# Kernel tuning notes

Measured on AMD Instinct MI355X. Metric: run time of the kernel, lower is better.

## Reference

```python
import jax, jax.numpy as jnp
import numpy as np
import math

D_MODEL = 1024
N_HEADS = 16
HEAD_DIM = D_MODEL // N_HEADS
BATCH = 2
SEQ = 2048


def setup_inputs() -> dict:
    key = jax.random.key(0)
    ks = jax.random.split(key, 6)
    x = jax.random.normal(ks[0], (BATCH, SEQ, D_MODEL), dtype=jnp.float32)
    # causal additive mask, finite large negative
    causal = jnp.tril(jnp.ones((SEQ, SEQ), dtype=bool))
    attn_mask = jnp.where(causal, 0.0, -1e9).astype(jnp.float32)[None, None, :, :]
    s = 1.0 / math.sqrt(D_MODEL)
    W_qkv = jax.random.uniform(ks[1], (3 * D_MODEL, D_MODEL), jnp.float32, -s, s)
    b_qkv = jax.random.uniform(ks[2], (3 * D_MODEL,), jnp.float32, -s, s)
    W_out = jax.random.uniform(ks[3], (D_MODEL, D_MODEL), jnp.float32, -s, s)
    b_out = jax.random.uniform(ks[4], (D_MODEL,), jnp.float32, -s, s)
    return {"x": x, "attn_mask": attn_mask, "W_qkv": W_qkv, "b_qkv": b_qkv,
            "W_out": W_out, "b_out": b_out}


def reference(x, attn_mask, W_qkv, b_qkv, W_out, b_out):
    batch, seq, _ = x.shape
    # torch Linear: x @ W^T + b
    qkv = x @ W_qkv.T + b_qkv                              # [B,S,3D]
    qkv = qkv.reshape(batch, seq, 3, N_HEADS, HEAD_DIM)
    qkv = jnp.transpose(qkv, (2, 0, 3, 1, 4))              # [3,B,H,S,hd]
    q, k, v = qkv[0], qkv[1], qkv[2]
    scores = jnp.einsum('bhsd,bhtd->bhst', q, k) / math.sqrt(HEAD_DIM)
    scores = scores + attn_mask
    attn = jax.nn.softmax(scores, axis=-1)                 # dropout p=0 (eval)
    context = jnp.einsum('bhst,bhtd->bhsd', attn, v)       # [B,H,S,hd]
    context = jnp.transpose(context, (0, 2, 1, 3)).reshape(batch, seq, D_MODEL)
    return context @ W_out.T + b_out
```

## Files before the change

kernel.cpp:

```cpp
#include <hip/hip_runtime.h>
#include <hip/hip_bf16.h>

#define BATCH 2
#define SEQ 2048
#define DMODEL 1024
#define NHEADS 16
#define HDIM 64
#define MROWS (BATCH*SEQ)

typedef short bf16x8_t __attribute__((ext_vector_type(8)));
typedef float f32x4_t __attribute__((ext_vector_type(4)));

union Frag { uint4 u; bf16x8_t b; };

__device__ __forceinline__ unsigned short f2bf(float f) {
  union { __hip_bfloat16 h; unsigned short s; } u;
  u.h = __float2bfloat16(f);
  return u.s;
}

__device__ __forceinline__ void gload16(const unsigned short* g, unsigned short* l) {
  __builtin_amdgcn_global_load_lds(
      (const __attribute__((address_space(1))) unsigned int*)(const void*)g,
      (__attribute__((address_space(3))) unsigned int*)(void*)l,
      16, 0, 0);
}

__global__ void cvt3_kernel(const float* __restrict__ a, const float* __restrict__ b,
                            const float* __restrict__ c,
                            unsigned short* __restrict__ oa, unsigned short* __restrict__ ob,
                            unsigned short* __restrict__ oc,
                            int na, int nb, int nc) {
  const int n = na + nb + nc;
  for (int i = blockIdx.x * blockDim.x + threadIdx.x; i < n;
       i += gridDim.x * blockDim.x) {
    const float* src; unsigned short* dst; int j;
    if (i < na)           { src = a; dst = oa; j = i; }
    else if (i < na + nb) { src = b; dst = ob; j = i - na; }
    else                  { src = c; dst = oc; j = i - na - nb; }
    float4 v = reinterpret_cast<const float4*>(src)[j];
    ushort4 o;
    o.x = f2bf(v.x); o.y = f2bf(v.y); o.z = f2bf(v.z); o.w = f2bf(v.w);
    reinterpret_cast<ushort4*>(dst)[j] = o;
  }
}

#define QSCALE 0.18033688011112042f


__launch_bounds__(256)
__global__ void qkv_gemm_kernel(const unsigned short* __restrict__ A,
                                const unsigned short* __restrict__ Bw,
                                const float* __restrict__ bias,
                                unsigned short* __restrict__ qb,
                                unsigned short* __restrict__ kb,
                                unsigned short* __restrict__ vb) {
  __shared__ __align__(16) unsigned short As[3 * 4096];
  __shared__ __align__(16) unsigned short Bs[3 * 4096];
  const int tid = threadIdx.x;
  const int w = tid >> 6, lane = tid & 63;
  const int rr = lane & 15, cg = lane >> 4;
  const int wr = w >> 1, wc = w & 1;
  const int kswz = (rr >> 1) & 3;
  const int bm = blockIdx.x * 128, bn = blockIdx.y * 128;

  const int cid0 = (w * 2) * 64 + lane, cid1 = (w * 2 + 1) * 64 + lane;
  const int rowA0 = cid0 >> 2, kc0 = (cid0 & 3) ^ ((cid0 >> 3) & 3);
  const int rowA1 = cid1 >> 2, kc1 = (cid1 & 3) ^ ((cid1 >> 3) & 3);
  const unsigned short* gA0 = A + (size_t)(bm + rowA0) * DMODEL + kc0 * 8;
  const unsigned short* gA1 = A + (size_t)(bm + rowA1) * DMODEL + kc1 * 8;
  const unsigned short* gB0 = Bw + (size_t)(bn + rowA0) * DMODEL + kc0 * 8;
  const unsigned short* gB1 = Bw + (size_t)(bn + rowA1) * DMODEL + kc1 * 8;
  unsigned short* lA0 = As + (w * 2) * 512;
  unsigned short* lA1 = As + (w * 2 + 1) * 512;
  unsigned short* lB0 = Bs + (w * 2) * 512;
  unsigned short* lB1 = Bs + (w * 2 + 1) * 512;

#define GSTAGE(bi_, k0_) do {                       \
    gload16(gA0 + (k0_), lA0 + (bi_) * 4096);       \
    gload16(gA1 + (k0_), lA1 + (bi_) * 4096);       \
    gload16(gB0 + (k0_), lB0 + (bi_) * 4096);       \
    gload16(gB1 + (k0_), lB1 + (bi_) * 4096);       \
  } while (0)

  f32x4_t acc[4][4];
#pragma unroll
  for (int i = 0; i < 4; ++i)
#pragma unroll
    for (int j = 0; j < 4; ++j) acc[i][j] = (f32x4_t){0.f, 0.f, 0.f, 0.f};

  GSTAGE(0, 0);
  GSTAGE(1, 32);
  int cur = 0;
  for (int it = 0; it < 32; ++it) {
    if (it < 31) asm volatile("s_waitcnt vmcnt(4)" ::: "memory");
    else         asm volatile("s_waitcnt vmcnt(0)" ::: "memory");
    __builtin_amdgcn_sched_barrier(0);
    __builtin_amdgcn_s_barrier();
    __builtin_amdgcn_sched_barrier(0);
    if (it + 2 < 32) {
      int nb2 = cur + 2; if (nb2 >= 3) nb2 -= 3;
      GSTAGE(nb2, (it + 2) * 32);
    }
    const uint4* A4 = reinterpret_cast<const uint4*>(As) + cur * 512;
    const uint4* B4 = reinterpret_cast<const uint4*>(Bs) + cur * 512;
    Frag af[4], bf[4];
#pragma unroll
    for (int mt = 0; mt < 4; ++mt)
      af[mt].u = A4[(wr * 64 + 16 * mt + rr) * 4 + (cg ^ kswz)];
#pragma unroll
    for (int nt = 0; nt < 4; ++nt)
      bf[nt].u = B4[(wc * 64 + 16 * nt + rr) * 4 + (cg ^ kswz)];
    __builtin_amdgcn_s_setprio(1);
#pragma unroll
    for (int mt = 0; mt < 4; ++mt)
#pragma unroll
      for (int nt = 0; nt < 4; ++nt)
        acc[mt][nt] = __builtin_amdgcn_mfma_f32_16x16x32_bf16(af[mt].b, bf[nt].b, acc[mt][nt], 0, 0, 0);
    __builtin_amdgcn_s_setprio(0);
    cur = (cur == 2) ? 0 : cur + 1;
  }
#undef GSTAGE

#pragma unroll
  for (int nt = 0; nt < 4; ++nt) {
    const int m = bn + wc * 64 + 16 * nt + rr;
    const float bv = bias[m];
    const int which = m >> 10;
    const int h = (m & 1023) >> 6;
    const int d = m & 63;
#pragma unroll
    for (int mt = 0; mt < 4; ++mt) {
#pragma unroll
      for (int r = 0; r < 4; ++r) {
        const int n = bm + wr * 64 + 16 * mt + cg * 4 + r;
        const int b = n >> 11, sq = n & (SEQ - 1);
        const int bh = b * NHEADS + h;
        float val = acc[mt][nt][r] + bv;
        if (which == 0) {
          qb[((size_t)bh * SEQ + sq) * HDIM + d] = f2bf(val * QSCALE);
        } else if (which == 1) {
          kb[((size_t)bh * SEQ + sq) * HDIM + d] = f2bf(val);
        } else {
          vb[((size_t)bh * HDIM + d) * SEQ + sq] = f2bf(val);
        }
      }
    }
  }
}

__launch_bounds__(256)
__global__ void out_gemm_kernel(const unsigned short* __restrict__ A,
                                const unsigned short* __restrict__ Bw,
                                const float* __restrict__ bias,
                                float* __restrict__ out) {
  __shared__ __align__(16) unsigned short As[3 * 4096];
  __shared__ __align__(16) unsigned short Bs[3 * 4096];
  const int tid = threadIdx.x;
  const int w = tid >> 6, lane = tid & 63;
  const int rr = lane & 15, cg = lane >> 4;
  const int wr = w >> 1, wc = w & 1;
  const int kswz = (rr >> 1) & 3;
  const int bm = blockIdx.x * 128, bn = blockIdx.y * 128;

  const int cid0 = (w * 2) * 64 + lane, cid1 = (w * 2 + 1) * 64 + lane;
  const int rowA0 = cid0 >> 2, kc0 = (cid0 & 3) ^ ((cid0 >> 3) & 3);
  const int rowA1 = cid1 >> 2, kc1 = (cid1 & 3) ^ ((cid1 >> 3) & 3);
  const unsigned short* gA0 = A + (size_t)(bm + rowA0) * DMODEL + kc0 * 8;
  const unsigned short* gA1 = A + (size_t)(bm + rowA1) * DMODEL + kc1 * 8;
  const unsigned short* gB0 = Bw + (size_t)(bn + rowA0) * DMODEL + kc0 * 8;
  const unsigned short* gB1 = Bw + (size_t)(bn + rowA1) * DMODEL + kc1 * 8;
  unsigned short* lA0 = As + (w * 2) * 512;
  unsigned short* lA1 = As + (w * 2 + 1) * 512;
  unsigned short* lB0 = Bs + (w * 2) * 512;
  unsigned short* lB1 = Bs + (w * 2 + 1) * 512;

#define GSTAGE(bi_, k0_) do {                       \
    gload16(gA0 + (k0_), lA0 + (bi_) * 4096);       \
    gload16(gA1 + (k0_), lA1 + (bi_) * 4096);       \
    gload16(gB0 + (k0_), lB0 + (bi_) * 4096);       \
    gload16(gB1 + (k0_), lB1 + (bi_) * 4096);       \
  } while (0)

  f32x4_t acc[4][4];
#pragma unroll
  for (int i = 0; i < 4; ++i)
#pragma unroll
    for (int j = 0; j < 4; ++j) acc[i][j] = (f32x4_t){0.f, 0.f, 0.f, 0.f};

  GSTAGE(0, 0);
  GSTAGE(1, 32);
  int cur = 0;
  for (int it = 0; it < 32; ++it) {
    if (it < 31) asm volatile("s_waitcnt vmcnt(4)" ::: "memory");
    else         asm volatile("s_waitcnt vmcnt(0)" ::: "memory");
    __builtin_amdgcn_sched_barrier(0);
    __builtin_amdgcn_s_barrier();
    __builtin_amdgcn_sched_barrier(0);
    if (it + 2 < 32) {
      int nb2 = cur + 2; if (nb2 >= 3) nb2 -= 3;
      GSTAGE(nb2, (it + 2) * 32);
    }
    const uint4* A4 = reinterpret_cast<const uint4*>(As) + cur * 512;
    const uint4* B4 = reinterpret_cast<const uint4*>(Bs) + cur * 512;
    Frag af[4], bf[4];
#pragma unroll
    for (int mt = 0; mt < 4; ++mt)
      af[mt].u = A4[(wr * 64 + 16 * mt + rr) * 4 + (cg ^ kswz)];
#pragma unroll
    for (int nt = 0; nt < 4; ++nt)
      bf[nt].u = B4[(wc * 64 + 16 * nt + rr) * 4 + (cg ^ kswz)];
    __builtin_amdgcn_s_setprio(1);
#pragma unroll
    for (int mt = 0; mt < 4; ++mt)
#pragma unroll
      for (int nt = 0; nt < 4; ++nt)
        acc[mt][nt] = __builtin_amdgcn_mfma_f32_16x16x32_bf16(af[mt].b, bf[nt].b, acc[mt][nt], 0, 0, 0);
    __builtin_amdgcn_s_setprio(0);
    cur = (cur == 2) ? 0 : cur + 1;
  }
#undef GSTAGE

#pragma unroll
  for (int nt = 0; nt < 4; ++nt) {
    const int m = bn + wc * 64 + 16 * nt + rr;
    const float bv = bias[m];
#pragma unroll
    for (int mt = 0; mt < 4; ++mt) {
#pragma unroll
      for (int r = 0; r < 4; ++r) {
        const int n = bm + wr * 64 + 16 * mt + cg * 4 + r;
        out[(size_t)n * DMODEL + m] = acc[mt][nt][r] + bv;
      }
    }
  }
}

__launch_bounds__(256, 4)
__global__ void attn_kernel(const unsigned short* __restrict__ qb,
                            const unsigned short* __restrict__ kb,
                            const unsigned short* __restrict__ vb,
                            unsigned short* __restrict__ ctx) {
  __shared__ __align__(16) uint4 Ks[2][512];
  __shared__ __align__(16) uint4 Vs[2][512];

  const int tid = threadIdx.x;
  const int w = tid >> 6, lane = tid & 63;
  const int rr = lane & 15, cg = lane >> 4;
  const int rxw = rr & 7;
  const int bh = blockIdx.x;
  const int c = 31 - blockIdx.y;

  const unsigned short* Kbh = kb + (size_t)bh * SEQ * HDIM;
  const unsigned short* Vbh = vb + (size_t)bh * HDIM * SEQ;

  const int j0 = w * 2, j1 = w * 2 + 1;
  const int cid0 = j0 * 64 + lane, cid1 = j1 * 64 + lane;
  const int row0 = cid0 >> 3, ch0 = cid0 & 7;
  const int row1 = cid1 >> 3, ch1 = cid1 & 7;
  const int kOff0 = row0 * HDIM + ((ch0 ^ (row0 & 7)) << 3);
  const int kOff1 = row1 * HDIM + ((ch1 ^ (row1 & 7)) << 3);
  const int vOff0 = row0 * SEQ + ((ch0 ^ (row0 & 7)) << 3);
  const int vOff1 = row1 * SEQ + ((ch1 ^ (row1 & 7)) << 3);

#define STAGE(bi, tb_) do {                                             \
    const unsigned short* Kt_ = Kbh + (size_t)(tb_) * HDIM;             \
    const unsigned short* Vt_ = Vbh + (tb_);                            \
    unsigned short* kl_ = (unsigned short*)&Ks[bi][0];                  \
    unsigned short* vl_ = (unsigned short*)&Vs[bi][0];                  \
    gload16(Kt_ + kOff0, kl_ + j0 * 512);                               \
    gload16(Kt_ + kOff1, kl_ + j1 * 512);                               \
    gload16(Vt_ + vOff0, vl_ + j0 * 512);                               \
    gload16(Vt_ + vOff1, vl_ + j1 * 512);                               \
  } while (0)

  const int b = bh >> 4, h = bh & 15;
  const int s_base = c * 64 + w * 16;
  const int nt = c + 1;

  STAGE(0, 0);

  Frag q0, q1;
  {
    const unsigned short* qrow = qb + ((size_t)bh * SEQ + (s_base + rr)) * HDIM;
    q0.u = *reinterpret_cast<const uint4*>(qrow + cg * 8);
    q1.u = *reinterpret_cast<const uint4*>(qrow + 32 + cg * 8);
  }

  f32x4_t acc[4];
#pragma unroll
  for (int i = 0; i < 4; ++i) acc[i] = (f32x4_t){0.f, 0.f, 0.f, 0.f};
  float mreg = -1e30f;
  float lp = 0.f;

  for (int t = 0; t < nt; ++t) {
    __syncthreads();
    if (t + 1 < nt) STAGE((t + 1) & 1, (t + 1) * 64);
    const uint4* Kt = &Ks[t & 1][0];
    const uint4* Vt = &Vs[t & 1][0];

    f32x4_t s[4];
    __builtin_amdgcn_s_setprio(1);
#pragma unroll
    for (int st = 0; st < 4; ++st) {
      s[st] = (f32x4_t){0.f, 0.f, 0.f, 0.f};
      Frag kf;
      kf.u = Kt[(st * 16 + rr) * 8 + (cg ^ rxw)];
      s[st] = __builtin_amdgcn_mfma_f32_16x16x32_bf16(kf.b, q0.b, s[st], 0, 0, 0);
      kf.u = Kt[(st * 16 + rr) * 8 + ((4 + cg) ^ rxw)];
      s[st] = __builtin_amdgcn_mfma_f32_16x16x32_bf16(kf.b, q1.b, s[st], 0, 0, 0);
    }
    __builtin_amdgcn_s_setprio(0);

    if (t == nt - 1) {
#pragma unroll
      for (int st = 0; st < 4; ++st)
#pragma unroll
        for (int r = 0; r < 4; ++r)
          if (st * 16 + cg * 4 + r > w * 16 + rr) s[st][r] = -1e30f;
    }

    float mx = s[0][0];
#pragma unroll
    for (int st = 0; st < 4; ++st)
#pragma unroll
      for (int r = 0; r < 4; ++r) mx = fmaxf(mx, s[st][r]);
    if (__any(mx > mreg + 11.0f)) {
      float m = fmaxf(mx, __shfl_xor(mx, 16));
      m = fmaxf(m, __shfl_xor(m, 32));
      m = fmaxf(m, mreg);
      const float alpha = exp2f(mreg - m);
      mreg = m;
      lp *= alpha;
      float av[4];
#pragma unroll
      for (int r = 0; r < 4; ++r) av[r] = __shfl(alpha, cg * 4 + r);
#pragma unroll
      for (int dt = 0; dt < 4; ++dt)
#pragma unroll
        for (int r = 0; r < 4; ++r) acc[dt][r] *= av[r];
    }

    float pv[4][4];
#pragma unroll
    for (int st = 0; st < 4; ++st)
#pragma unroll
      for (int r = 0; r < 4; ++r) {
        pv[st][r] = exp2f(s[st][r] - mreg);
        lp += pv[st][r];
      }

    unsigned int uu[4][2];
#pragma unroll
    for (int st = 0; st < 4; ++st)
#pragma unroll
      for (int i = 0; i < 2; ++i)
        asm("v_cvt_pk_bf16_f32 %0, %1, %2"
            : "=v"(uu[st][i]) : "v"(pv[st][2 * i]), "v"(pv[st][2 * i + 1]));

    Frag pA0, pA1;
#pragma unroll
    for (int s2 = 0; s2 < 2; ++s2) {
#pragma unroll
      for (int i = 0; i < 2; ++i) {
        unsigned int x = uu[2 * s2][i], y = uu[2 * s2 + 1][i];
        asm("v_permlane32_swap_b32 %0, %1" : "+v"(x), "+v"(y));
        asm("v_permlane16_swap_b32 %0, %1" : "+v"(x), "+v"(y));
        if (s2 == 0) { pA0.u[i] = x; pA0.u[2 + i] = y; }
        else         { pA1.u[i] = x; pA1.u[2 + i] = y; }
      }
    }

    __builtin_amdgcn_s_setprio(1);
#pragma unroll
    for (int dt = 0; dt < 4; ++dt) {
      Frag vf;
      vf.u = Vt[(dt * 16 + rr) * 8 + (cg ^ rxw)];
      acc[dt] = __builtin_amdgcn_mfma_f32_16x16x32_bf16(pA0.b, vf.b, acc[dt], 0, 0, 0);
      vf.u = Vt[(dt * 16 + rr) * 8 + ((4 + cg) ^ rxw)];
      acc[dt] = __builtin_amdgcn_mfma_f32_16x16x32_bf16(pA1.b, vf.b, acc[dt], 0, 0, 0);
    }
    __builtin_amdgcn_s_setprio(0);
  }

  float ls = lp + __shfl_xor(lp, 16);
  ls += __shfl_xor(ls, 32);
  const float inv = 1.0f / ls;
  float iv[4];
#pragma unroll
  for (int r = 0; r < 4; ++r) iv[r] = __shfl(inv, cg * 4 + r);
#pragma unroll
  for (int r = 0; r < 4; ++r) {
    const int sq = s_base + cg * 4 + r;
    unsigned short* crow = ctx + (size_t)(b * SEQ + sq) * DMODEL + h * HDIM;
#pragma unroll
    for (int dt = 0; dt < 4; ++dt)
      crow[dt * 16 + rr] = f2bf(acc[dt][r] * iv[r]);
  }
#undef STAGE
}

extern "C" void kernel_launch(void* const* d_in, const int* in_sizes, int n_in,
                              void* d_out, int out_size, void* d_ws, size_t ws_size,
                              hipStream_t stream) {
  const float* x    = (const float*)d_in[0];
  const float* Wqkv = (const float*)d_in[2];
  const float* bqkv = (const float*)d_in[3];
  const float* Wout = (const float*)d_in[4];
  const float* bout = (const float*)d_in[5];
  float* out = (float*)d_out;

  unsigned short* ws    = (unsigned short*)d_ws;
  unsigned short* xb    = ws;
  unsigned short* wqkvb = xb + (size_t)MROWS * DMODEL;
  unsigned short* woutb = wqkvb + (size_t)3 * DMODEL * DMODEL;
  unsigned short* qbuf  = woutb + (size_t)DMODEL * DMODEL;
  unsigned short* kbuf  = qbuf + (size_t)BATCH * NHEADS * SEQ * HDIM;
  unsigned short* vbuf  = kbuf + (size_t)BATCH * NHEADS * SEQ * HDIM;
  unsigned short* ctx   = vbuf + (size_t)BATCH * NHEADS * SEQ * HDIM;

  cvt3_kernel<<<2048, 256, 0, stream>>>(
      x, Wqkv, Wout, xb, wqkvb, woutb,
      MROWS * DMODEL / 4, 3 * DMODEL * DMODEL / 4, DMODEL * DMODEL / 4);

  qkv_gemm_kernel<<<dim3(MROWS / 128, 3 * DMODEL / 128), 256, 0, stream>>>(
      xb, wqkvb, bqkv, qbuf, kbuf, vbuf);

  attn_kernel<<<dim3(BATCH * NHEADS, SEQ / 64), 256, 0, stream>>>(
      qbuf, kbuf, vbuf, ctx);

  out_gemm_kernel<<<dim3(MROWS / 128, DMODEL / 128), 256, 0, stream>>>(
      ctx, woutb, bout, out);
}
```

Before: 111.4 us.

## Split long causal attention rows into KV segments with a combine pass

Query chunks with many key tiles are split into segments of up to 8 tiles. Each segment runs in its own block and writes an unnormalized partial output plus its row max and row sum. A new combine kernel merges the partials with log-sum-exp rescaling. This balances causal work across more blocks (80 per head instead of 32) and shortens the critical path, at the cost of an extra launch, extra global traffic for partials, and bf16 rounding of the partial outputs.

After: 121.5 us. 9.1% more time.

```diff
diff --git a/kernel.cpp b/kernel.cpp
--- a/kernel.cpp
+++ b/kernel.cpp
@@ -7,6 +7,7 @@
 #define NHEADS 16
 #define HDIM 64
 #define MROWS (BATCH*SEQ)
+#define PSLOTS 72
 
 typedef short bf16x8_t __attribute__((ext_vector_type(8)));
 typedef float f32x4_t __attribute__((ext_vector_type(4)));
@@ -17,6 +18,13 @@
   union { __hip_bfloat16 h; unsigned short s; } u;
   u.h = __float2bfloat16(f);
   return u.s;
+}
+
+__device__ __forceinline__ float bflo(unsigned int v) {
+  return __uint_as_float(v << 16);
+}
+__device__ __forceinline__ float bfhi(unsigned int v) {
+  return __uint_as_float(v & 0xffff0000u);
 }
 
 __device__ __forceinline__ void gload16(const unsigned short* g, unsigned short* l) {
@@ -240,7 +248,10 @@
 __global__ void attn_kernel(const unsigned short* __restrict__ qb,
                             const unsigned short* __restrict__ kb,
                             const unsigned short* __restrict__ vb,
-                            unsigned short* __restrict__ ctx) {
+                            unsigned short* __restrict__ ctx,
+                            unsigned short* __restrict__ pO,
+                            float* __restrict__ pm,
+                            float* __restrict__ pl) {
   __shared__ __align__(16) uint4 Ks[2][512];
   __shared__ __align__(16) uint4 Vs[2][512];
 
@@ -248,8 +259,18 @@
   const int w = tid >> 6, lane = tid & 63;
   const int rr = lane & 15, cg = lane >> 4;
   const int rxw = rr & 7;
-  const int bh = blockIdx.x;
-  const int c = 31 - blockIdx.y;
+  const int g = 79 - blockIdx.x;
+  const int bh = blockIdx.y;
+
+  int c, s;
+  if (g < 8)       { c = g;                  s = 0; }
+  else if (g < 24) { c = 8 + ((g - 8) >> 1); s = (g - 8) & 1; }
+  else if (g < 48) { c = 16 + (g - 24) / 3;  s = (g - 24) % 3; }
+  else             { c = 24 + ((g - 48) >> 2); s = (g - 48) & 3; }
+  const bool direct = (g < 8);
+  const int pslot = bh * PSLOTS + (g - 8);
+  const int t0 = s * 8;
+  const int t1 = min(t0 + 8, c + 1);
 
   const unsigned short* Kbh = kb + (size_t)bh * SEQ * HDIM;
   const unsigned short* Vbh = vb + (size_t)bh * HDIM * SEQ;
@@ -276,9 +297,8 @@
 
   const int b = bh >> 4, h = bh & 15;
   const int s_base = c * 64 + w * 16;
-  const int nt = c + 1;
-
-  STAGE(0, 0);
+
+  STAGE(t0 & 1, t0 * 64);
 
   Frag q0, q1;
   {
@@ -293,38 +313,38 @@
   float mreg = -1e30f;
   float lp = 0.f;
 
-  for (int t = 0; t < nt; ++t) {
+  for (int t = t0; t < t1; ++t) {
     __syncthreads();
-    if (t + 1 < nt) STAGE((t + 1) & 1, (t + 1) * 64);
+    if (t + 1 < t1) STAGE((t + 1) & 1, (t + 1) * 64);
     const uint4* Kt = &Ks[t & 1][0];
     const uint4* Vt = &Vs[t & 1][0];
 
-    f32x4_t s[4];
+    f32x4_t sc[4];
     __builtin_amdgcn_s_setprio(1);
 #pragma unroll
     for (int st = 0; st < 4; ++st) {
-      s[st] = (f32x4_t){0.f, 0.f, 0.f, 0.f};
+      sc[st] = (f32x4_t){0.f, 0.f, 0.f, 0.f};
       Frag kf;
       kf.u = Kt[(st * 16 + rr) * 8 + (cg ^ rxw)];
-      s[st] = __builtin_amdgcn_mfma_f32_16x16x32_bf16(kf.b, q0.b, s[st], 0, 0, 0);
+      sc[st] = __builtin_amdgcn_mfma_f32_16x16x32_bf16(kf.b, q0.b, sc[st], 0, 0, 0);
       kf.u = Kt[(st * 16 + rr) * 8 + ((4 + cg) ^ rxw)];
-      s[st] = __builtin_amdgcn_mfma_f32_16x16x32_bf16(kf.b, q1.b, s[st], 0, 0, 0);
+      sc[st] = __builtin_amdgcn_mfma_f32_16x16x32_bf16(kf.b, q1.b, sc[st], 0, 0, 0);
     }
     __builtin_amdgcn_s_setprio(0);
 
-    if (t == nt - 1) {
+    if (t == c) {
 #pragma unroll
       for (int st = 0; st < 4; ++st)
 #pragma unroll
         for (int r = 0; r < 4; ++r)
-          if (st * 16 + cg * 4 + r > w * 16 + rr) s[st][r] = -1e30f;
-    }
-
-    float mx = s[0][0];
+          if (st * 16 + cg * 4 + r > w * 16 + rr) sc[st][r] = -1e30f;
+    }
+
+    float mx = sc[0][0];
 #pragma unroll
     for (int st = 0; st < 4; ++st)
 #pragma unroll
-      for (int r = 0; r < 4; ++r) mx = fmaxf(mx, s[st][r]);
+      for (int r = 0; r < 4; ++r) mx = fmaxf(mx, sc[st][r]);
     if (__any(mx > mreg + 11.0f)) {
       float m = fmaxf(mx, __shfl_xor(mx, 16));
       m = fmaxf(m, __shfl_xor(m, 32));
@@ -346,7 +366,7 @@
     for (int st = 0; st < 4; ++st)
 #pragma unroll
       for (int r = 0; r < 4; ++r) {
-        pv[st][r] = exp2f(s[st][r] - mreg);
+        pv[st][r] = exp2f(sc[st][r] - mreg);
         lp += pv[st][r];
       }
 
@@ -385,19 +405,102 @@
 
   float ls = lp + __shfl_xor(lp, 16);
   ls += __shfl_xor(ls, 32);
-  const float inv = 1.0f / ls;
-  float iv[4];
-#pragma unroll
-  for (int r = 0; r < 4; ++r) iv[r] = __shfl(inv, cg * 4 + r);
-#pragma unroll
-  for (int r = 0; r < 4; ++r) {
-    const int sq = s_base + cg * 4 + r;
-    unsigned short* crow = ctx + (size_t)(b * SEQ + sq) * DMODEL + h * HDIM;
-#pragma unroll
-    for (int dt = 0; dt < 4; ++dt)
-      crow[dt * 16 + rr] = f2bf(acc[dt][r] * iv[r]);
+  if (direct) {
+    const float inv = 1.0f / ls;
+    float iv[4];
+#pragma unroll
+    for (int r = 0; r < 4; ++r) iv[r] = __shfl(inv, cg * 4 + r);
+#pragma unroll
+    for (int r = 0; r < 4; ++r) {
+      const int sq = s_base + cg * 4 + r;
+      unsigned short* crow = ctx + (size_t)(b * SEQ + sq) * DMODEL + h * HDIM;
+#pragma unroll
+      for (int dt = 0; dt < 4; ++dt)
+        crow[dt * 16 + rr] = f2bf(acc[dt][r] * iv[r]);
+    }
+  } else {
+    if (cg == 0) {
+      pm[(size_t)pslot * 64 + w * 16 + rr] = mreg;
+      pl[(size_t)pslot * 64 + w * 16 + rr] = ls;
+    }
+    unsigned short* Ob = pO + (size_t)pslot * 4096;
+#pragma unroll
+    for (int r = 0; r < 4; ++r) {
+      const int row = w * 16 + cg * 4 + r;
+#pragma unroll
+      for (int dt = 0; dt < 4; ++dt)
+        Ob[row * 64 + dt * 16 + rr] = f2bf(acc[dt][r]);
+    }
   }
 #undef STAGE
+}
+
+__launch_bounds__(256)
+__global__ void combine_kernel(const unsigned short* __restrict__ pO,
+                               const float* __restrict__ pm,
+                               const float* __restrict__ pl,
+                               unsigned short* __restrict__ ctx) {
+  const int c = 8 + blockIdx.x;
+  const int bh = blockIdx.y;
+  const int b = bh >> 4, h = bh & 15;
+  const int nseg = (c + 8) >> 3;
+  const int base = (c < 16) ? 2 * (c - 8)
+                 : (c < 24) ? 16 + 3 * (c - 16)
+                            : 40 + 4 * (c - 24);
+  const int tid = threadIdx.x;
+  const int row = tid >> 2;
+  const int d0 = (tid & 3) * 16;
+
+  const size_t slot0 = (size_t)bh * PSLOTS + base;
+
+  float mv[4], lv[4];
+  float mstar = -1e30f;
+  for (int i = 0; i < nseg; ++i) {
+    mv[i] = pm[(slot0 + i) * 64 + row];
+    lv[i] = pl[(slot0 + i) * 64 + row];
+    mstar = fmaxf(mstar, mv[i]);
+  }
+  float lstar = 0.f;
+  float wgt[4];
+  for (int i = 0; i < nseg; ++i) {
+    wgt[i] = exp2f(mv[i] - mstar);
+    lstar += lv[i] * wgt[i];
+  }
+  const float inv = 1.0f / lstar;
+
+  float o[16];
+#pragma unroll
+  for (int j = 0; j < 16; ++j) o[j] = 0.f;
+  for (int i = 0; i < nseg; ++i) {
+    const uint4* src = reinterpret_cast<const uint4*>(
+        pO + (slot0 + i) * 4096 + row * 64 + d0);
+    uint4 u0 = src[0], u1 = src[1];
+    const float wi = wgt[i];
+    o[0]  += bflo(u0.x) * wi; o[1]  += bfhi(u0.x) * wi;
+    o[2]  += bflo(u0.y) * wi; o[3]  += bfhi(u0.y) * wi;
+    o[4]  += bflo(u0.z) * wi; o[5]  += bfhi(u0.z) * wi;
+    o[6]  += bflo(u0.w) * wi; o[7]  += bfhi(u0.w) * wi;
+    o[8]  += bflo(u1.x) * wi; o[9]  += bfhi(u1.x) * wi;
+    o[10] += bflo(u1.y) * wi; o[11] += bfhi(u1.y) * wi;
+    o[12] += bflo(u1.z) * wi; o[13] += bfhi(u1.z) * wi;
+    o[14] += bflo(u1.w) * wi; o[15] += bfhi(u1.w) * wi;
+  }
+
+  ushort4 w0, w1, w2, w3;
+  w0.x = f2bf(o[0] * inv);  w0.y = f2bf(o[1] * inv);
+  w0.z = f2bf(o[2] * inv);  w0.w = f2bf(o[3] * inv);
+  w1.x = f2bf(o[4] * inv);  w1.y = f2bf(o[5] * inv);
+  w1.z = f2bf(o[6] * inv);  w1.w = f2bf(o[7] * inv);
+  w2.x = f2bf(o[8] * inv);  w2.y = f2bf(o[9] * inv);
+  w2.z = f2bf(o[10] * inv); w2.w = f2bf(o[11] * inv);
+  w3.x = f2bf(o[12] * inv); w3.y = f2bf(o[13] * inv);
+  w3.z = f2bf(o[14] * inv); w3.w = f2bf(o[15] * inv);
+
+  unsigned short* dst = ctx + (size_t)(b * SEQ + c * 64 + row) * DMODEL + h * HDIM + d0;
+  reinterpret_cast<ushort4*>(dst)[0] = w0;
+  reinterpret_cast<ushort4*>(dst)[1] = w1;
+  reinterpret_cast<ushort4*>(dst)[2] = w2;
+  reinterpret_cast<ushort4*>(dst)[3] = w3;
 }
 
 extern "C" void kernel_launch(void* const* d_in, const int* in_sizes, int n_in,
@@ -418,6 +521,9 @@
   unsigned short* kbuf  = qbuf + (size_t)BATCH * NHEADS * SEQ * HDIM;
   unsigned short* vbuf  = kbuf + (size_t)BATCH * NHEADS * SEQ * HDIM;
   unsigned short* ctx   = vbuf + (size_t)BATCH * NHEADS * SEQ * HDIM;
+  unsigned short* pO    = ctx + (size_t)MROWS * DMODEL;
+  float* pm = (float*)(pO + (size_t)32 * PSLOTS * 4096);
+  float* pl = pm + (size_t)32 * PSLOTS * 64;
 
   cvt3_kernel<<<2048, 256, 0, stream>>>(
       x, Wqkv, Wout, xb, wqkvb, woutb,
@@ -426,8 +532,11 @@
   qkv_gemm_kernel<<<dim3(MROWS / 128, 3 * DMODEL / 128), 256, 0, stream>>>(
       xb, wqkvb, bqkv, qbuf, kbuf, vbuf);
 
-  attn_kernel<<<dim3(BATCH * NHEADS, SEQ / 64), 256, 0, stream>>>(
-      qbuf, kbuf, vbuf, ctx);
+  attn_kernel<<<dim3(80, BATCH * NHEADS), 256, 0, stream>>>(
+      qbuf, kbuf, vbuf, ctx, pO, pm, pl);
+
+  combine_kernel<<<dim3(24, BATCH * NHEADS), 256, 0, stream>>>(
+      pO, pm, pl, ctx);
 
   out_gemm_kernel<<<dim3(MROWS / 128, DMODEL / 128), 256, 0, stream>>>(
       ctx, woutb, bout, out);
```
